# Kernel optimization log

Measured on AMD Instinct MI355X. Metric: run time of the kernel, lower is better.

The kernel has to match this reference:

```python
import jax, jax.numpy as jnp
import numpy as np

D_MODEL = 768
NUM_HEADS = 12
D_K = D_MODEL // NUM_HEADS
D_FF = 3072
EPS = 1e-5


def _layer_norm(x, gamma, beta):
    mu = jnp.mean(x, axis=-1, keepdims=True)
    var = jnp.mean(jnp.square(x - mu), axis=-1, keepdims=True)
    return (x - mu) * jax.lax.rsqrt(var + EPS) * gamma + beta


def setup_inputs() -> dict:
    key = jax.random.key(0)
    ks = jax.random.split(key, 16)
    s = 1.0 / np.sqrt(D_MODEL)
    sf = 1.0 / np.sqrt(D_FF)
    inp = {
        "x": jax.random.normal(ks[0], (2, 2048, D_MODEL), dtype=jnp.float32),
        "Wq": jax.random.uniform(ks[1], (D_MODEL, D_MODEL), jnp.float32, -s, s),
        "bq": jax.random.uniform(ks[2], (D_MODEL,), jnp.float32, -s, s),
        "Wk": jax.random.uniform(ks[3], (D_MODEL, D_MODEL), jnp.float32, -s, s),
        "bk": jax.random.uniform(ks[4], (D_MODEL,), jnp.float32, -s, s),
        "Wv": jax.random.uniform(ks[5], (D_MODEL, D_MODEL), jnp.float32, -s, s),
        "bv": jax.random.uniform(ks[6], (D_MODEL,), jnp.float32, -s, s),
        "Wo": jax.random.uniform(ks[7], (D_MODEL, D_MODEL), jnp.float32, -s, s),
        "bo": jax.random.uniform(ks[8], (D_MODEL,), jnp.float32, -s, s),
        "W1": jax.random.uniform(ks[9], (D_MODEL, D_FF), jnp.float32, -s, s),
        "b1": jax.random.uniform(ks[10], (D_FF,), jnp.float32, -s, s),
        "W2": jax.random.uniform(ks[11], (D_FF, D_MODEL), jnp.float32, -sf, sf),
        "b2": jax.random.uniform(ks[12], (D_MODEL,), jnp.float32, -sf, sf),
        "g1": jnp.ones((D_MODEL,), jnp.float32),
        "be1": jnp.zeros((D_MODEL,), jnp.float32),
        "g2": jnp.ones((D_MODEL,), jnp.float32),
        "be2": jnp.zeros((D_MODEL,), jnp.float32),
    }
    return inp


def reference(x, Wq, bq, Wk, bk, Wv, bv, Wo, bo, W1, b1, W2, b2, g1, be1, g2, be2):
    B, S, _ = x.shape

    def split(h):  # (B,S,D) -> (B,H,S,Dk)
        return h.reshape(B, S, NUM_HEADS, D_K).transpose(0, 2, 1, 3)

    q = split(x @ Wq + bq)
    k = split(x @ Wk + bk)
    v = split(x @ Wv + bv)

    # naive attention: materialize full (B,H,S,S) scores as in the original
    scores = jnp.einsum("bhsd,bhtd->bhst", q, k) / np.sqrt(D_K)
    attn = jax.nn.softmax(scores, axis=-1)
    ctx = jnp.einsum("bhst,bhtd->bhsd", attn, v)
    ctx = ctx.transpose(0, 2, 1, 3).reshape(B, S, D_MODEL)
    attn_out = ctx @ Wo + bo

    x = _layer_norm(x + attn_out, g1, be1)
    ff = jax.nn.relu(x @ W1 + b1) @ W2 + b2
    x = _layer_norm(x + ff, g2, be2)
    return x
```

## Files before the change

### kernel.cpp

```cpp
#include <hip/hip_runtime.h>
#include <cstdint>


typedef unsigned short u16;
typedef unsigned int u32;
typedef __attribute__((ext_vector_type(4))) float f32x4;
typedef __attribute__((ext_vector_type(8))) short s16x8;
typedef __attribute__((ext_vector_type(4))) u16  u16x4;
typedef __attribute__((ext_vector_type(2))) u32  u32x2;

#define AS1 __attribute__((address_space(1)))
#define AS3 __attribute__((address_space(3)))

__device__ __forceinline__ u16 f2b(float f) {
  union { float f; unsigned u; } v; v.f = f;
  unsigned r = v.u + 0x7FFFu + ((v.u >> 16) & 1u);
  return (u16)(r >> 16);
}

__device__ __forceinline__ float b2f(u16 v) {
  union { float f; u32 u; } x; x.u = ((u32)v) << 16; return x.f;
}

__device__ __forceinline__ void gl_lds16(const void* g, void* lds_uniform_base) {
  __builtin_amdgcn_global_load_lds((const AS1 void*)g, (AS3 void*)lds_uniform_base, 16, 0, 0);
}

__device__ __forceinline__ f32x4 mfma16(s16x8 a, s16x8 b, f32x4 c) {
  return __builtin_amdgcn_mfma_f32_16x16x32_bf16(a, b, c, 0, 0, 0);
}

__device__ __forceinline__ u32 cvt_pk_bf16(float lo, float hi) {
  u32 r;
  asm("v_cvt_pk_bf16_f32 %0, %1, %2" : "=v"(r) : "v"(lo), "v"(hi));
  return r;
}

__device__ __forceinline__ float max3f(float a, float b, float c) {
  return fmaxf(fmaxf(a, b), c);
}

__device__ __forceinline__ void block_barrier() {
  asm volatile("" ::: "memory");
  __builtin_amdgcn_s_barrier();
  asm volatile("" ::: "memory");
}

__global__ __launch_bounds__(256) void prep(
    const float* __restrict__ Wq, const float* __restrict__ Wk,
    const float* __restrict__ Wv, const float* __restrict__ Wo,
    const float* __restrict__ W1, const float* __restrict__ W2,
    const float* __restrict__ bq, const float* __restrict__ bk,
    const float* __restrict__ bv, const float* __restrict__ x,
    u16* __restrict__ Wqkv_t, u16* __restrict__ Wo_t,
    u16* __restrict__ W1_t, u16* __restrict__ W2_t,
    float* __restrict__ bqkv, u16* __restrict__ Xb, int convBlocks) {
  __shared__ float ts[32][33];
  const int bid = blockIdx.x;
  const int tx = threadIdx.x, ty = threadIdx.y;
  if (bid < 6912) {
    const float* W; u16* Wt; int K, N, tile;
    if (bid < 2304) {
      int w = bid / 576; tile = bid - w * 576; K = 768; N = 768;
      W = (w == 0) ? Wq : (w == 1) ? Wk : (w == 2) ? Wv : Wo;
      Wt = (w < 3) ? Wqkv_t + (size_t)w * 768 * 768 : Wo_t;
    } else if (bid < 4608) {
      tile = bid - 2304; K = 768; N = 3072; W = W1; Wt = W1_t;
    } else {
      tile = bid - 4608; K = 3072; N = 768; W = W2; Wt = W2_t;
    }
    int ntx = N >> 5;
    int n0 = (tile % ntx) * 32, k0 = (tile / ntx) * 32;
#pragma unroll
    for (int yy = 0; yy < 32; yy += 8)
      ts[ty + yy][tx] = W[(size_t)(k0 + ty + yy) * N + n0 + tx];
    __syncthreads();
#pragma unroll
    for (int yy = 0; yy < 32; yy += 8)
      Wt[(size_t)(n0 + ty + yy) * K + k0 + tx] = f2b(ts[tx][ty + yy]);
  } else if (bid < 6912 + convBlocks) {
    int t = ty * 32 + tx;
    size_t i = ((size_t)(bid - 6912) * 256 + t) * 4;
    f32x4 v = *(const f32x4*)(x + i);
    u16x4 o;
#pragma unroll
    for (int k = 0; k < 4; ++k) o[k] = f2b(v[k]);
    *(u16x4*)(Xb + i) = o;
  } else {
    int t = ty * 32 + tx;
    int i = (bid - 6912 - convBlocks) * 256 + t;
    if (i < 2304) bqkv[i] = (i < 768) ? bq[i] : (i < 1536) ? bk[i - 768] : bv[i - 1536];
  }
}

template <int MODE>
__global__ __launch_bounds__(256) void gemm_bt(const u16* __restrict__ A,
                                               const u16* __restrict__ Bt,
                                               const float* __restrict__ bias,
                                               u16* __restrict__ Cb,
                                               u16* __restrict__ Qo, u16* __restrict__ Ko,
                                               u16* __restrict__ Vt, int M, int N, int K,
                                               int Klen) {
  __shared__ __align__(16) u16 lsA[2][128 * 64];
  __shared__ __align__(16) u16 lsB[2][128 * 64];
  const int tid = threadIdx.x;
  const int lane = tid & 63, wave = tid >> 6;
  const int lr = lane & 15, lh = lane >> 4;
  const int wr = wave >> 1, wc = wave & 1;

  int bx, by, bz;
  {
    int nx = gridDim.x, ny = gridDim.y, nz = gridDim.z;
    int total = nx * ny * nz;
    int lin = blockIdx.x + nx * (blockIdx.y + ny * blockIdx.z);
    if ((total & 7) == 0) {
      int key = (lin & 7) * (total >> 3) + (lin >> 3);
      by = key % ny;
      int t2 = key / ny;
      bz = t2 % nz;
      bx = t2 / nz;
    } else {
      bx = blockIdx.x; by = blockIdx.y; bz = blockIdx.z;
    }
  }
  const int m0 = by * 128;
  const int n0 = bx * 128;
  const int kB = bz * Klen;

  f32x4 acc[4][4];
#pragma unroll
  for (int i = 0; i < 4; ++i)
#pragma unroll
    for (int j = 0; j < 4; ++j) acc[i][j] = f32x4{0.f, 0.f, 0.f, 0.f};

  const size_t aBase = (size_t)m0 * K;
  const size_t bBase = (size_t)n0 * K;
  const int srow8 = tid >> 3;
  const int scolE = (((tid & 7) * 16) ^ ((srow8 & 7) << 4)) >> 1;
  const int xk = (lr & 7) << 4;

  auto stage = [&](int buf, int kt) {
#pragma unroll
    for (int i = 0; i < 4; ++i) {
      int row = i * 32 + srow8;
      int ldsOff = buf * 16384 + i * 4096 + wave * 1024;
      gl_lds16(A + aBase + (size_t)row * K + kt + scolE, (char*)lsA + ldsOff);
      gl_lds16(Bt + bBase + (size_t)row * K + kt + scolE, (char*)lsB + ldsOff);
    }
  };

  const int nk = Klen >> 6;
  stage(0, kB);
  for (int t = 0; t < nk; ++t) {
    const int cur = t & 1;
    if (t + 1 < nk) {
      stage(cur ^ 1, kB + (t + 1) * 64);
      asm volatile("s_waitcnt vmcnt(8)" ::: "memory");
    } else {
      asm volatile("s_waitcnt vmcnt(0)" ::: "memory");
    }
    block_barrier();
    const char* baA = (const char*)lsA + cur * 16384;
    const char* baB = (const char*)lsB + cur * 16384;
#pragma unroll
    for (int ks = 0; ks < 2; ++ks) {
      int cb = (ks * 64 + lh * 16) ^ xk;
      s16x8 a[4], b[4];
#pragma unroll
      for (int i = 0; i < 4; ++i) {
        a[i] = *(const s16x8*)(baA + (wr * 64 + i * 16 + lr) * 128 + cb);
        b[i] = *(const s16x8*)(baB + (wc * 64 + i * 16 + lr) * 128 + cb);
      }
#pragma unroll
      for (int i = 0; i < 4; ++i)
#pragma unroll
        for (int j = 0; j < 4; ++j) acc[i][j] = mfma16(a[i], b[j], acc[i][j]);
    }
    block_barrier();
  }

  u16* CbP = Cb + (size_t)bz * M * N;
#pragma unroll
  for (int i = 0; i < 4; ++i) {
    int growb = m0 + wr * 64 + i * 16 + lh * 4;
#pragma unroll
    for (int j = 0; j < 4; ++j) {
      int col = n0 + wc * 64 + j * 16 + lr;
      float bv = (MODE != 0 || bz == 0) ? bias[col] : 0.f;
      if (MODE == 2) {
        int sel = col / 768;
        int c2 = col - sel * 768;
        int h = c2 >> 6, d = c2 & 63;
        int b = growb >> 11, s0 = growb & 2047;
        if (sel == 2) {
          u16x4 ob;
#pragma unroll
          for (int q = 0; q < 4; ++q) ob[q] = f2b(acc[i][j][q] + bv);
          *(u16x4*)(Vt + (((size_t)(b * 12 + h)) * 64 + d) * 2048 + s0) = ob;
        } else {
#pragma unroll
          for (int q = 0; q < 4; ++q) {
            float v = acc[i][j][q] + bv;
            size_t idx = (((size_t)(b * 12 + h)) * 2048 + (s0 + q)) * 64 + d;
            float vv = (sel == 0) ? v * 0.1803368801f : v;
            u16* dst = (sel == 0) ? Qo : Ko;
            dst[idx] = f2b(vv);
          }
        }
      } else {
#pragma unroll
        for (int q = 0; q < 4; ++q) {
          int grow = growb + q;
          float v = acc[i][j][q] + bv;
          if (MODE == 0) {
            CbP[(size_t)grow * N + col] = f2b(v);
          } else {
            Cb[(size_t)grow * N + col] = f2b(fmaxf(v, 0.f));
          }
        }
      }
    }
  }
}

__global__ __launch_bounds__(512) void attn(const u16* __restrict__ Qh,
                                            const u16* __restrict__ Kh,
                                            const u16* __restrict__ Vt,
                                            u16* __restrict__ Opb,
                                            float* __restrict__ ml,
                                            int nbh, int ntile) {
  __shared__ __align__(16) u16 lsK[2][64 * 64];
  __shared__ __align__(16) u16 lsV[2][64 * 64];
  __shared__ __align__(16) u16 lsP[8][16 * 64];
  const int tid = threadIdx.x, lane = tid & 63, wave = tid >> 6;
  const int lr = lane & 15, lh = lane >> 4;

  int bx = blockIdx.x, bh = blockIdx.y, z = blockIdx.z;
  {
    int nz = gridDim.z;
    int total = 16 * nbh * nz;
    if ((total & 7) == 0) {
      int lin = bx + 16 * (bh + nbh * z);
      int nl = (lin & 7) * (total >> 3) + (lin >> 3);
      bx = nl & 15;
      bh = (nl >> 4) % nbh;
      z = nl / (16 * nbh);
    }
  }
  const int q0 = bx * 128 + wave * 16;
  const size_t kvBase = (size_t)bh * 2048 * 64;
  const int tB = z * ntile;

  const int srow = tid >> 3;
  const int scol = (((tid & 7) * 16) ^ ((srow & 7) << 4)) >> 1;
  const u16* kSrcBase = Kh + kvBase + (size_t)srow * 64 + scol;
  const u16* vSrcBase = Vt + kvBase + (size_t)srow * 2048 + scol;

  s16x8 qf[2];
#pragma unroll
  for (int ks = 0; ks < 2; ++ks)
    qf[ks] = *(const s16x8*)(Qh + kvBase + (size_t)(q0 + lr) * 64 + ks * 32 + lh * 8);

  s16x8 onesf;
#pragma unroll
  for (int k = 0; k < 8; ++k) onesf[k] = (short)0x3F80;

  f32x4 oacc[4];
  f32x4 aOnes = f32x4{0.f, 0.f, 0.f, 0.f};
  float mrow = -1e30f;
#pragma unroll
  for (int d = 0; d < 4; ++d) oacc[d] = f32x4{0.f, 0.f, 0.f, 0.f};

  gl_lds16(kSrcBase + (size_t)tB * 4096, (char*)lsK[0] + wave * 1024);
  gl_lds16(vSrcBase + tB * 64,           (char*)lsV[0] + wave * 1024);

  for (int it = 0; it < ntile; ++it) {
    const int cur = it & 1;
    __syncthreads();

    s16x8 kb[2][4];
#pragma unroll
    for (int ks = 0; ks < 2; ++ks)
#pragma unroll
      for (int j = 0; j < 4; ++j) {
        int r = j * 16 + lr;
        kb[ks][j] = *(const s16x8*)((const char*)lsK[cur] + r * 128 +
                                    ((ks * 64 + lh * 16) ^ ((r & 7) << 4)));
      }

    if (it + 1 < ntile) {
      int t = tB + it + 1;
      gl_lds16(kSrcBase + (size_t)t * 4096, (char*)lsK[cur ^ 1] + wave * 1024);
      gl_lds16(vSrcBase + t * 64,           (char*)lsV[cur ^ 1] + wave * 1024);
    }

    f32x4 st[4];
#pragma unroll
    for (int j = 0; j < 4; ++j) st[j] = f32x4{0.f, 0.f, 0.f, 0.f};
    __builtin_amdgcn_s_setprio(1);
#pragma unroll
    for (int ks = 0; ks < 2; ++ks)
#pragma unroll
      for (int j = 0; j < 4; ++j) st[j] = mfma16(kb[ks][j], qf[ks], st[j]);
    __builtin_amdgcn_s_setprio(0);

    float mx;
    {
      float t0 = max3f(st[0][0], st[0][1], st[0][2]);
      float t1 = max3f(st[0][3], st[1][0], st[1][1]);
      float t2 = max3f(st[1][2], st[1][3], st[2][0]);
      float t3 = max3f(st[2][1], st[2][2], st[2][3]);
      float t4 = max3f(st[3][0], st[3][1], st[3][2]);
      mx = fmaxf(max3f(t0, t1, t2), max3f(t3, t4, st[3][3]));
      mx = fmaxf(mx, __shfl_xor(mx, 16));
      mx = fmaxf(mx, __shfl_xor(mx, 32));
    }
    if (__any(mx > mrow + 11.f)) {
      float mn = fmaxf(mrow, mx);
      float al = exp2f(mrow - mn);
      mrow = mn;
#pragma unroll
      for (int q = 0; q < 4; ++q) aOnes[q] *= al;
#pragma unroll
      for (int d = 0; d < 4; ++d)
#pragma unroll
        for (int q = 0; q < 4; ++q) oacc[d][q] *= al;
    }

#pragma unroll
    for (int j = 0; j < 4; ++j) {
      float p0 = exp2f(st[j][0] - mrow);
      float p1 = exp2f(st[j][1] - mrow);
      float p2 = exp2f(st[j][2] - mrow);
      float p3 = exp2f(st[j][3] - mrow);
      u32x2 pk;
      pk.x = cvt_pk_bf16(p0, p1);
      pk.y = cvt_pk_bf16(p2, p3);
      *(u32x2*)((char*)lsP[wave] + lr * 128 + ((j * 32 + lh * 8) ^ ((lr & 7) << 4))) = pk;
    }

    __builtin_amdgcn_s_setprio(1);
#pragma unroll
    for (int ks = 0; ks < 2; ++ks) {
      s16x8 pa = *(const s16x8*)((const char*)lsP[wave] + lr * 128 +
                                 ((ks * 64 + lh * 16) ^ ((lr & 7) << 4)));
      aOnes = mfma16(onesf, pa, aOnes);
#pragma unroll
      for (int d = 0; d < 4; ++d) {
        int r = d * 16 + lr;
        s16x8 vb = *(const s16x8*)((const char*)lsV[cur] + r * 128 +
                                   ((ks * 64 + lh * 16) ^ ((r & 7) << 4)));
        oacc[d] = mfma16(vb, pa, oacc[d]);
      }
    }
    __builtin_amdgcn_s_setprio(0);
  }

  {
    int s = q0 + lr;
    size_t r = ((size_t)z * nbh + bh) * 2048 + s;
#pragma unroll
    for (int d = 0; d < 4; ++d) {
      u32x2 pk;
      pk.x = cvt_pk_bf16(oacc[d][0], oacc[d][1]);
      pk.y = cvt_pk_bf16(oacc[d][2], oacc[d][3]);
      *(u32x2*)(Opb + r * 64 + d * 16 + lh * 4) = pk;
    }
    if (lh == 0) { ml[r * 2] = mrow; ml[r * 2 + 1] = aOnes[0]; }
  }
}

template <int NZ>
__global__ __launch_bounds__(256) void attn_combine(const u16* __restrict__ Opb,
                                                    const float* __restrict__ ml,
                                                    u16* __restrict__ ctx, int nbh) {
  size_t i = (size_t)blockIdx.x * 256 + threadIdx.x;
  int d4 = (int)(i & 15);
  size_t rs = i >> 4;
  size_t zs = (size_t)nbh * 2048;
  float m[NZ], l[NZ];
  float mx = -1e30f;
#pragma unroll
  for (int p = 0; p < NZ; ++p) {
    m[p] = ml[(p * zs + rs) * 2];
    l[p] = ml[(p * zs + rs) * 2 + 1];
    mx = fmaxf(mx, m[p]);
  }
  float wsum = 0.f, a[NZ];
#pragma unroll
  for (int p = 0; p < NZ; ++p) { a[p] = exp2f(m[p] - mx); wsum += l[p] * a[p]; }
  float inv = 1.f / wsum;
  f32x4 o = f32x4{0.f, 0.f, 0.f, 0.f};
#pragma unroll
  for (int p = 0; p < NZ; ++p) {
    u16x4 op = *(const u16x4*)(Opb + (p * zs + rs) * 64 + d4 * 4);
#pragma unroll
    for (int k = 0; k < 4; ++k) o[k] += b2f(op[k]) * a[p];
  }
  int bh = (int)(rs >> 11), s = (int)(rs & 2047);
  int b = bh / 12, h = bh - b * 12;
  u16x4 r;
#pragma unroll
  for (int k = 0; k < 4; ++k) r[k] = f2b(o[k] * inv);
  *(u16x4*)(ctx + ((size_t)(b * 2048 + s)) * 768 + h * 64 + d4 * 4) = r;
}

template <int NP, int XBF>
__global__ __launch_bounds__(256) void resid_ln(const void* __restrict__ xin,
                                                const u16* __restrict__ yp,
                                                size_t pstride,
                                                const float* __restrict__ gamma,
                                                const float* __restrict__ beta,
                                                float* __restrict__ outf,
                                                u16* __restrict__ outb) {
  const int row = blockIdx.x, t = threadIdx.x;
  const size_t base4 = (size_t)row * 192;
  const bool act = t < 192;
  f32x4 v = f32x4{0.f, 0.f, 0.f, 0.f};
  float s = 0.f, s2 = 0.f;
  if (act) {
    if (XBF) {
      u16x4 xv = *(const u16x4*)((const u16*)xin + (size_t)row * 768 + t * 4);
#pragma unroll
      for (int k = 0; k < 4; ++k) v[k] = b2f(xv[k]);
    } else {
      v = ((const f32x4*)xin)[base4 + t];
    }
#pragma unroll
    for (int p = 0; p < NP; ++p) {
      u16x4 y = *(const u16x4*)(yp + p * pstride + (size_t)row * 768 + t * 4);
#pragma unroll
      for (int k = 0; k < 4; ++k) v[k] += b2f(y[k]);
    }
    s = (v[0] + v[1]) + (v[2] + v[3]);
    s2 = (v[0] * v[0] + v[1] * v[1]) + (v[2] * v[2] + v[3] * v[3]);
  }
#pragma unroll
  for (int off = 32; off > 0; off >>= 1) {
    s += __shfl_down(s, off, 64);
    s2 += __shfl_down(s2, off, 64);
  }
  __shared__ float red[8];
  int lane = t & 63, wave = t >> 6;
  if (lane == 0) { red[wave] = s; red[4 + wave] = s2; }
  __syncthreads();
  s = red[0] + red[1] + red[2] + red[3];
  s2 = red[4] + red[5] + red[6] + red[7];
  const float inv = 1.f / 768.f;
  float mu = s * inv;
  float var = fmaxf(s2 * inv - mu * mu, 0.f);
  float rs = rsqrtf(var + 1e-5f);
  if (act) {
    f32x4 g = ((const f32x4*)gamma)[t];
    f32x4 bb = ((const f32x4*)beta)[t];
    f32x4 o;
#pragma unroll
    for (int k = 0; k < 4; ++k) o[k] = (v[k] - mu) * rs * g[k] + bb[k];
    if (outf) ((f32x4*)outf)[base4 + t] = o;
    if (outb) {
      u16x4 ob;
#pragma unroll
      for (int k = 0; k < 4; ++k) ob[k] = f2b(o[k]);
      ((u16x4*)outb)[base4 + t] = ob;
    }
  }
}

extern "C" void kernel_launch(void* const* d_in, const int* in_sizes, int n_in,
                              void* d_out, int out_size, void* d_ws, size_t ws_size,
                              hipStream_t stream) {
  const float* x   = (const float*)d_in[0];
  const float* Wq  = (const float*)d_in[1];
  const float* bq  = (const float*)d_in[2];
  const float* Wk  = (const float*)d_in[3];
  const float* bk  = (const float*)d_in[4];
  const float* Wv  = (const float*)d_in[5];
  const float* bv  = (const float*)d_in[6];
  const float* Wo  = (const float*)d_in[7];
  const float* bo  = (const float*)d_in[8];
  const float* W1  = (const float*)d_in[9];
  const float* b1  = (const float*)d_in[10];
  const float* W2  = (const float*)d_in[11];
  const float* b2  = (const float*)d_in[12];
  const float* g1  = (const float*)d_in[13];
  const float* be1 = (const float*)d_in[14];
  const float* g2  = (const float*)d_in[15];
  const float* be2 = (const float*)d_in[16];
  float* out = (float*)d_out;

  const int M = in_sizes[0] / 768;
  const int B = M / 2048;
  const int nbh = B * 12;

  char* ws = (char*)d_ws;
  size_t off = 0;
  auto alloc = [&](size_t bytes) -> void* {
    void* p = ws + off;
    off += (bytes + 255) & ~(size_t)255;
    return p;
  };
  u16*   Wqkv_t = (u16*)alloc((size_t)2304 * 768 * 2);
  u16*   Wo_t   = (u16*)alloc((size_t)768 * 768 * 2);
  u16*   W1_t   = (u16*)alloc((size_t)3072 * 768 * 2);
  u16*   W2_t   = (u16*)alloc((size_t)768 * 3072 * 2);
  float* bqkv   = (float*)alloc(2304 * 4);
  u16*   Xb     = (u16*)alloc((size_t)M * 768 * 2);
  u16*   Qh     = (u16*)alloc((size_t)M * 768 * 2);
  u16*   Kh     = (u16*)alloc((size_t)M * 768 * 2);
  u16*   Vt     = (u16*)alloc((size_t)M * 768 * 2);

  size_t pstride = (size_t)M * 768;
  size_t fixedRest = pstride * 2  +
                     (size_t)M * 3072 * 2  + 4096;
  const int ZSPLIT = 2;
  size_t opElems = (size_t)ZSPLIT * nbh * 2048 * 64;
  size_t attnBytes = opElems * 2 + (size_t)ZSPLIT * nbh * 2048 * 2 * 4;
  size_t reg4 = attnBytes;
  if (reg4 < pstride * 2 * 4) reg4 = pstride * 2 * 4;
  int FSPLIT;
  size_t regionBytes;
  if (off + reg4 + fixedRest <= ws_size) {
    FSPLIT = 4; regionBytes = reg4;
  } else {
    FSPLIT = 2;
    regionBytes = attnBytes > pstride * 2 * 2 ? attnBytes : pstride * 2 * 2;
  }
  float* region = (float*)alloc(regionBytes);
  u16*   Opb  = (u16*)region;
  float* ml   = (float*)((char*)region + opElems * 2);
  u16*   projPart = (u16*)region;
  u16*   ffnPart  = (u16*)region;
  u16*   x1b  = (u16*)alloc(pstride * 2);
  u16*   hb   = (u16*)alloc((size_t)M * 3072 * 2);
  u16*   ctx  = Xb;

  dim3 tb(32, 8);
  const int convBlocks = (M * 768) / 1024;
  prep<<<6912 + convBlocks + 9, tb, 0, stream>>>(
      Wq, Wk, Wv, Wo, W1, W2, bq, bk, bv, x,
      Wqkv_t, Wo_t, W1_t, W2_t, bqkv, Xb, convBlocks);

  gemm_bt<2><<<dim3(2304 / 128, M / 128), 256, 0, stream>>>(
      Xb, Wqkv_t, bqkv, nullptr, Qh, Kh, Vt, M, 2304, 768, 768);

  attn<<<dim3(16, nbh, ZSPLIT), 512, 0, stream>>>(Qh, Kh, Vt, Opb, ml, nbh, 32 / ZSPLIT);
  attn_combine<2><<<nbh * 128, 256, 0, stream>>>(Opb, ml, ctx, nbh);

  gemm_bt<0><<<dim3(768 / 128, M / 128, 2), 256, 0, stream>>>(
      ctx, Wo_t, bo, projPart, nullptr, nullptr, nullptr, M, 768, 768, 384);

  resid_ln<2, 0><<<M, 256, 0, stream>>>(x, projPart, pstride, g1, be1,
                                        nullptr, x1b);

  gemm_bt<1><<<dim3(3072 / 128, M / 128), 256, 0, stream>>>(
      x1b, W1_t, b1, hb, nullptr, nullptr, nullptr, M, 3072, 768, 768);

  if (FSPLIT == 4) {
    gemm_bt<0><<<dim3(768 / 128, M / 128, 4), 256, 0, stream>>>(
        hb, W2_t, b2, ffnPart, nullptr, nullptr, nullptr, M, 768, 3072, 768);
    resid_ln<4, 1><<<M, 256, 0, stream>>>(x1b, ffnPart, pstride, g2, be2,
                                          out, nullptr);
  } else {
    gemm_bt<0><<<dim3(768 / 128, M / 128, 2), 256, 0, stream>>>(
        hb, W2_t, b2, ffnPart, nullptr, nullptr, nullptr, M, 768, 3072, 1536);
    resid_ln<2, 1><<<M, 256, 0, stream>>>(x1b, ffnPart, pstride, g2, be2,
                                          out, nullptr);
  }
}
```

Before: 200.6 us.

## Replace split-K output GEMMs with 64-row tile GEMM writing full results

Adds a gemm_m64 kernel that uses 64x128 tiles with no K split, and uses it for the Wo projection and the W2 FFN GEMM instead of split-K gemm_bt with partial buffers. The residual-layernorm kernels now read one full-precision-summed bf16 result instead of summing 2 or 4 partials, which cuts partial-buffer traffic and reduction work. Smaller M tiles keep enough blocks to fill the GPU without split-K. The trade-off is longer per-block K loops (3072 for W2) and lower per-block reuse of the B tile.

```diff
diff --git a/kernel.cpp b/kernel.cpp
--- a/kernel.cpp
+++ b/kernel.cpp
@@ -223,6 +223,101 @@
   }
 }
 
+__global__ __launch_bounds__(256) void gemm_m64(const u16* __restrict__ A,
+                                                const u16* __restrict__ Bt,
+                                                const float* __restrict__ bias,
+                                                u16* __restrict__ Cb,
+                                                int M, int N, int K) {
+  __shared__ __align__(16) u16 lsA[2][64 * 64];
+  __shared__ __align__(16) u16 lsB[2][128 * 64];
+  const int tid = threadIdx.x;
+  const int lane = tid & 63, wave = tid >> 6;
+  const int lr = lane & 15, lh = lane >> 4;
+
+  int bx, by;
+  {
+    int nx = gridDim.x, ny = gridDim.y;
+    int total = nx * ny;
+    int lin = blockIdx.x + nx * blockIdx.y;
+    if ((total & 7) == 0) {
+      int key = (lin & 7) * (total >> 3) + (lin >> 3);
+      by = key % ny;
+      bx = key / ny;
+    } else {
+      bx = blockIdx.x; by = blockIdx.y;
+    }
+  }
+  const int m0 = by * 64;
+  const int n0 = bx * 128;
+
+  f32x4 acc[4][2];
+#pragma unroll
+  for (int i = 0; i < 4; ++i)
+#pragma unroll
+    for (int j = 0; j < 2; ++j) acc[i][j] = f32x4{0.f, 0.f, 0.f, 0.f};
+
+  const size_t aBase = (size_t)m0 * K;
+  const size_t bBase = (size_t)n0 * K;
+  const int srow8 = tid >> 3;
+  const int scolE = (((tid & 7) * 16) ^ ((srow8 & 7) << 4)) >> 1;
+  const int xk = (lr & 7) << 4;
+
+  auto stage = [&](int buf, int kt) {
+#pragma unroll
+    for (int i = 0; i < 2; ++i)
+      gl_lds16(A + aBase + (size_t)(i * 32 + srow8) * K + kt + scolE,
+               (char*)lsA + buf * 8192 + i * 4096 + wave * 1024);
+#pragma unroll
+    for (int i = 0; i < 4; ++i)
+      gl_lds16(Bt + bBase + (size_t)(i * 32 + srow8) * K + kt + scolE,
+               (char*)lsB + buf * 16384 + i * 4096 + wave * 1024);
+  };
+
+  const int nk = K >> 6;
+  stage(0, 0);
+  for (int t = 0; t < nk; ++t) {
+    const int cur = t & 1;
+    if (t + 1 < nk) {
+      stage(cur ^ 1, (t + 1) * 64);
+      asm volatile("s_waitcnt vmcnt(6)" ::: "memory");
+    } else {
+      asm volatile("s_waitcnt vmcnt(0)" ::: "memory");
+    }
+    block_barrier();
+    const char* baA = (const char*)lsA + cur * 8192;
+    const char* baB = (const char*)lsB + cur * 16384;
+#pragma unroll
+    for (int ks = 0; ks < 2; ++ks) {
+      int cb = (ks * 64 + lh * 16) ^ xk;
+      s16x8 a[4], b[2];
+#pragma unroll
+      for (int i = 0; i < 4; ++i)
+        a[i] = *(const s16x8*)(baA + (i * 16 + lr) * 128 + cb);
+#pragma unroll
+      for (int j = 0; j < 2; ++j)
+        b[j] = *(const s16x8*)(baB + (wave * 32 + j * 16 + lr) * 128 + cb);
+#pragma unroll
+      for (int i = 0; i < 4; ++i)
+#pragma unroll
+        for (int j = 0; j < 2; ++j) acc[i][j] = mfma16(a[i], b[j], acc[i][j]);
+    }
+    block_barrier();
+  }
+
+#pragma unroll
+  for (int i = 0; i < 4; ++i) {
+    int growb = m0 + i * 16 + lh * 4;
+#pragma unroll
+    for (int j = 0; j < 2; ++j) {
+      int col = n0 + wave * 32 + j * 16 + lr;
+      float bv = bias[col];
+#pragma unroll
+      for (int q = 0; q < 4; ++q)
+        Cb[(size_t)(growb + q) * N + col] = f2b(acc[i][j][q] + bv);
+    }
+  }
+}
+
 __global__ __launch_bounds__(512) void attn(const u16* __restrict__ Qh,
                                             const u16* __restrict__ Kh,
                                             const u16* __restrict__ Vt,
@@ -510,26 +605,15 @@
   u16*   Vt     = (u16*)alloc((size_t)M * 768 * 2);
 
   size_t pstride = (size_t)M * 768;
-  size_t fixedRest = pstride * 2  +
-                     (size_t)M * 3072 * 2  + 4096;
   const int ZSPLIT = 2;
   size_t opElems = (size_t)ZSPLIT * nbh * 2048 * 64;
   size_t attnBytes = opElems * 2 + (size_t)ZSPLIT * nbh * 2048 * 2 * 4;
-  size_t reg4 = attnBytes;
-  if (reg4 < pstride * 2 * 4) reg4 = pstride * 2 * 4;
-  int FSPLIT;
-  size_t regionBytes;
-  if (off + reg4 + fixedRest <= ws_size) {
-    FSPLIT = 4; regionBytes = reg4;
-  } else {
-    FSPLIT = 2;
-    regionBytes = attnBytes > pstride * 2 * 2 ? attnBytes : pstride * 2 * 2;
-  }
+  size_t regionBytes = attnBytes > pstride * 2 ? attnBytes : pstride * 2;
   float* region = (float*)alloc(regionBytes);
   u16*   Opb  = (u16*)region;
   float* ml   = (float*)((char*)region + opElems * 2);
-  u16*   projPart = (u16*)region;
-  u16*   ffnPart  = (u16*)region;
+  u16*   projFull = Qh;
+  u16*   ffnFull  = (u16*)region;
   u16*   x1b  = (u16*)alloc(pstride * 2);
   u16*   hb   = (u16*)alloc((size_t)M * 3072 * 2);
   u16*   ctx  = Xb;
@@ -546,24 +630,18 @@
   attn<<<dim3(16, nbh, ZSPLIT), 512, 0, stream>>>(Qh, Kh, Vt, Opb, ml, nbh, 32 / ZSPLIT);
   attn_combine<2><<<nbh * 128, 256, 0, stream>>>(Opb, ml, ctx, nbh);
 
-  gemm_bt<0><<<dim3(768 / 128, M / 128, 2), 256, 0, stream>>>(
-      ctx, Wo_t, bo, projPart, nullptr, nullptr, nullptr, M, 768, 768, 384);
-
-  resid_ln<2, 0><<<M, 256, 0, stream>>>(x, projPart, pstride, g1, be1,
+  gemm_m64<<<dim3(768 / 128, M / 64), 256, 0, stream>>>(
+      ctx, Wo_t, bo, projFull, M, 768, 768);
+
+  resid_ln<1, 0><<<M, 256, 0, stream>>>(x, projFull, pstride, g1, be1,
                                         nullptr, x1b);
 
   gemm_bt<1><<<dim3(3072 / 128, M / 128), 256, 0, stream>>>(
       x1b, W1_t, b1, hb, nullptr, nullptr, nullptr, M, 3072, 768, 768);
 
-  if (FSPLIT == 4) {
-    gemm_bt<0><<<dim3(768 / 128, M / 128, 4), 256, 0, stream>>>(
-        hb, W2_t, b2, ffnPart, nullptr, nullptr, nullptr, M, 768, 3072, 768);
-    resid_ln<4, 1><<<M, 256, 0, stream>>>(x1b, ffnPart, pstride, g2, be2,
-                                          out, nullptr);
-  } else {
-    gemm_bt<0><<<dim3(768 / 128, M / 128, 2), 256, 0, stream>>>(
-        hb, W2_t, b2, ffnPart, nullptr, nullptr, nullptr, M, 768, 3072, 1536);
-    resid_ln<2, 1><<<M, 256, 0, stream>>>(x1b, ffnPart, pstride, g2, be2,
-                                          out, nullptr);
-  }
-}
+  gemm_m64<<<dim3(768 / 128, M / 64), 256, 0, stream>>>(
+      hb, W2_t, b2, ffnFull, M, 768, 3072);
+
+  resid_ln<1, 1><<<M, 256, 0, stream>>>(x1b, ffnFull, pstride, g2, be2,
+                                        out, nullptr);
+}
```

Measured after the change: 200.8 us. About the same (+0.1%).
